# Kernel tuning notes

Measured on AMD Instinct MI355X. Metric: run time of the kernel, lower is better.

## Reference

```python
import jax, jax.numpy as jnp
import numpy as np
from jax import lax

K = 8  # number of KNN neighbors (excluding self)


def setup_inputs() -> dict:
    key = jax.random.key(0)
    k1, k2, k3 = jax.random.split(key, 3)
    B, H, W, C = 32, 14, 14, 2048
    OUT = 512
    x = jax.random.normal(k1, (B, H, W, C), dtype=jnp.float32)
    W1 = jax.random.normal(k2, (C, OUT), dtype=jnp.float32) * (1.0 / np.sqrt(C))
    b1 = jnp.zeros((OUT,), dtype=jnp.float32)
    W2 = jax.random.normal(k3, (OUT, OUT), dtype=jnp.float32) * (1.0 / np.sqrt(OUT))
    b2 = jnp.zeros((OUT,), dtype=jnp.float32)
    return {"x": x, "W1": W1, "b1": b1, "W2": W2, "b2": b2}


def _knn_edges(xf, k):
    # full pairwise squared-euclidean distance (monotone in cdist p=2)
    sq = jnp.sum(xf * xf, axis=-1)                      # [N]
    d2 = sq[:, None] + sq[None, :] - 2.0 * (xf @ xf.T)  # [N, N]
    _, idx = lax.top_k(-d2, k + 1)                      # smallest k+1
    knn = idx[:, 1:]                                    # drop self
    N = xf.shape[0]
    src = jnp.repeat(jnp.arange(N), k)
    dst = knn.reshape(-1)
    # GCNConv adds self-loops
    loops = jnp.arange(N)
    src = jnp.concatenate([src, loops])
    dst = jnp.concatenate([dst, loops])
    return src, dst


def _gcn_conv(h, W, b, src, dst, N):
    # PyG GCNConv: sym-normalized aggregation with self-loops
    deg = jax.ops.segment_sum(jnp.ones_like(dst, dtype=h.dtype), dst, num_segments=N)
    dinv = lax.rsqrt(jnp.maximum(deg, 1.0))
    norm = dinv[src] * dinv[dst]                        # [E]
    hw = h @ W                                          # [N, F]
    msg = hw[src] * norm[:, None]                       # gather + scale
    out = jax.ops.segment_sum(msg, dst, num_segments=N) # scatter-add
    return out + b


def reference(x, W1, b1, W2, b2):
    B, H, Wd, C = x.shape
    N = B * H * Wd
    xf = x.reshape(N, C)
    src, dst = _knn_edges(xf, K)
    h = jax.nn.relu(_gcn_conv(xf, W1, b1, src, dst, N))
    # dropout is identity in eval mode
    h = jax.nn.relu(_gcn_conv(h, W2, b2, src, dst, N))
    return h.reshape(B, H, Wd, W2.shape[1])
```

## Files before the change

### kernel.cpp

```cpp
#include <hip/hip_runtime.h>

typedef __attribute__((ext_vector_type(8))) _Float16 half8;
typedef __attribute__((ext_vector_type(4))) _Float16 half4;
typedef __attribute__((ext_vector_type(4))) float f32x4;

#define N_NODES 6272
#define CDIM    2048
#define ODIM    512
#define NPAN    49
#define NSLOT   392
#define GRID_G  1232
#define GRID_H1 392
#define E2      0.5f

#define XHI_OFF    0ul
#define CANDV_OFF  25690112ul
#define CANDI_OFF  35524608ul
#define SQ_OFF     40441856ul
#define KNN_OFF    40466944ul
#define DINV_OFF   41520640ul
#define RPTR_OFF   41545728ul
#define COL_OFF    41571072ul
#define W1T_OFF    41796864ul
#define W2T_OFF    43894016ul
#define H1H_OFF    44418304ul
#define HW_OFF     50843648ul

__device__ __forceinline__ void gld_lds16(const void* g, void* l) {
    __builtin_amdgcn_global_load_lds(
        (const __attribute__((address_space(1))) void*)g,
        (__attribute__((address_space(3))) void*)l, 16, 0, 0);
}

__device__ __forceinline__ half8 frag_read(const char* base, int row, int s, int lane) {
    int b = (s * 4 + (lane >> 4)) ^ (row & 7);
    return *(const half8*)(base + row * 128 + b * 16);
}

#define MF(a, b, c) __builtin_amdgcn_mfma_f32_16x16x32_f16(a, b, c, 0, 0, 0)

__global__ __launch_bounds__(256) void prep_kernel(const float* __restrict__ x,
        _Float16* __restrict__ xhi, float* __restrict__ sq,
        const float* __restrict__ W1, _Float16* __restrict__ w1t,
        const float* __restrict__ W2, _Float16* __restrict__ w2t) {
    __shared__ float tile[64][65];
    int bid = blockIdx.x, tid = threadIdx.x;
    if (bid < 1568) {
        int i = bid * 4 + (tid >> 6);
        int t = tid & 63;
        const float* row = x + (size_t)i * CDIM;
        _Float16* hrow = xhi + (size_t)i * CDIM;
        float s = 0.f;
#pragma unroll
        for (int k = 0; k < 8; k++) {
            float4 v = *(const float4*)(row + (k * 64 + t) * 4);
            half4 h;
            h[0] = (_Float16)v.x; h[1] = (_Float16)v.y;
            h[2] = (_Float16)v.z; h[3] = (_Float16)v.w;
            *(half4*)(hrow + (k * 64 + t) * 4) = h;
            s += v.x * v.x + v.y * v.y + v.z * v.z + v.w * v.w;
        }
#pragma unroll
        for (int off = 32; off; off >>= 1) s += __shfl_down(s, off, 64);
        if (t == 0) sq[i] = s;
        return;
    }
    const float* W; _Float16* Wt; int K, N, idx;
    if (bid < 1824) { idx = bid - 1568; W = W1; Wt = w1t; K = CDIM; N = ODIM; }
    else            { idx = bid - 1824; W = W2; Wt = w2t; K = ODIM; N = ODIM; }
    int nkb = K / 64;
    int kb = (idx % nkb) * 64, nb = (idx / nkb) * 64;
    int r = tid >> 2, c0 = (tid & 3) * 16;
#pragma unroll
    for (int u = 0; u < 4; u++) {
        float4 v = *(const float4*)(W + (size_t)(kb + r) * N + nb + c0 + u * 4);
        tile[r][c0 + u * 4 + 0] = v.x; tile[r][c0 + u * 4 + 1] = v.y;
        tile[r][c0 + u * 4 + 2] = v.z; tile[r][c0 + u * 4 + 3] = v.w;
    }
    __syncthreads();
    int rn = tid >> 2, ck0 = (tid & 3) * 16;
#pragma unroll
    for (int u = 0; u < 4; u++) {
        half4 o;
#pragma unroll
        for (int j = 0; j < 4; j++) o[j] = (_Float16)tile[ck0 + u * 4 + j][rn];
        *(half4*)(Wt + (size_t)(nb + rn) * K + kb + ck0 + u * 4) = o;
    }
}

__global__ __launch_bounds__(256, 4) void gram_hgemm_kernel(
        const _Float16* __restrict__ xhi, const float* __restrict__ sq,
        float* __restrict__ candv, unsigned short* __restrict__ candi,
        const _Float16* __restrict__ w1t, _Float16* __restrict__ hw) {
    __shared__ char lds[32768];
    int tid = threadIdx.x, lane = tid & 63, wave = tid >> 6;
    int l15 = lane & 15, kg = lane >> 4;
    int r_in = lane >> 3;
    int skb = (lane & 7) ^ r_in;

    if (blockIdx.x >= GRID_G) {
        int hb = blockIdx.x - GRID_G;
        const int nit = N_NODES / 64;
        int per = GRID_H1 >> 3;
        int swz = (hb & 7) * per + (hb >> 3);
        int i0 = (swz % nit) * 64, j0 = (swz / nit) * 128;
        f32x4 acc[4][2] = {};
#pragma unroll 1
        for (int kk = 0; kk < CDIM; kk += 64) {
            __syncthreads();
#pragma unroll
            for (int g = 0; g < 6; g++) {
                int sg = wave * 6 + g;
                if (sg < 8) {
                    gld_lds16(xhi + (size_t)(i0 + sg * 8 + r_in) * CDIM + kk + skb * 8,
                              lds + sg * 1024);
                } else {
                    int seg = sg - 8;
                    gld_lds16(w1t + (size_t)(j0 + seg * 8 + r_in) * CDIM + kk + skb * 8,
                              lds + 8192 + seg * 1024);
                }
            }
            __syncthreads();
#pragma unroll
            for (int s = 0; s < 2; s++) {
                half8 a[4];
#pragma unroll
                for (int m = 0; m < 4; m++) a[m] = frag_read(lds, m * 16 + l15, s, lane);
#pragma unroll
                for (int n = 0; n < 2; n++) {
                    half8 b = frag_read(lds + 8192, wave * 32 + n * 16 + l15, s, lane);
#pragma unroll
                    for (int m = 0; m < 4; m++) acc[m][n] = MF(a[m], b, acc[m][n]);
                }
            }
        }
#pragma unroll
        for (int m = 0; m < 4; m++)
#pragma unroll
            for (int n = 0; n < 2; n++)
#pragma unroll
                for (int r = 0; r < 4; r++) {
                    int row = i0 + m * 16 + kg * 4 + r;
                    int colj = j0 + wave * 32 + n * 16 + l15;
                    hw[(size_t)row * ODIM + colj] = (_Float16)acc[m][n][r];
                }
        return;
    }

    float* S = (float*)lds;
    float* topv = (float*)(lds + 16896);
    unsigned short* topi = (unsigned short*)(lds + 21504);
#define TOPV(r, k) topv[(r) * 9 + (k)]
#define TOPI(r, k) topi[(r) * 10 + (k)]
    int wr = wave >> 1, wc = wave & 1;

    int xcd = blockIdx.x & 7, loc = blockIdx.x >> 3;
    if (xcd != 0 && loc >= 153) return;
    int raster = (xcd == 0) ? loc : (154 + (xcd - 1) * 153 + loc);
    int t = (int)((sqrtf(8.f * (float)raster + 1.f) - 1.f) * 0.5f);
    while ((t + 1) * (t + 2) / 2 <= raster) t++;
    while (t * (t + 1) / 2 > raster) t--;
    int p = raster - t * (t + 1) / 2;
    size_t i0 = (size_t)p * 128, j0 = (size_t)t * 128;

    f32x4 acc[4][4] = {};

#pragma unroll 1
    for (int c = 0; c < 32; c++) {
        int kk = c * 64;
#pragma unroll
        for (int g = 0; g < 8; g++) {
            int sg = wave * 8 + g;
            int tI = sg >> 4, seg = sg & 15;
            size_t row = (tI ? j0 : i0) + (size_t)(seg * 8 + r_in);
            gld_lds16(xhi + row * CDIM + kk + skb * 8, lds + tI * 16384 + seg * 1024);
        }
        __syncthreads();
#pragma unroll
        for (int s = 0; s < 2; s++) {
            half8 a4[4];
#pragma unroll
            for (int m = 0; m < 4; m++)
                a4[m] = frag_read(lds, wr * 64 + m * 16 + l15, s, lane);
#pragma unroll
            for (int n = 0; n < 4; n++) {
                half8 b = frag_read(lds + 16384, wc * 64 + n * 16 + l15, s, lane);
#pragma unroll
                for (int m = 0; m < 4; m++) acc[m][n] = MF(a4[m], b, acc[m][n]);
            }
        }
        __syncthreads();
    }

    float sqi[4][4];
#pragma unroll
    for (int m = 0; m < 4; m++)
#pragma unroll
        for (int r = 0; r < 4; r++)
            sqi[m][r] = sq[(int)i0 + wr * 64 + m * 16 + kg * 4 + r];
    float sqj[4];
#pragma unroll
    for (int n = 0; n < 4; n++)
        sqj[n] = sq[(int)j0 + wc * 64 + n * 16 + l15];

    if (tid < 128) {
#pragma unroll
        for (int k = 0; k < 8; k++) { TOPV(tid, k) = 3.4e38f; TOPI(tid, k) = 0xFFFF; }
    }

#pragma unroll
    for (int cs = 0; cs < 4; cs++) {
        __syncthreads();
        if (wc == (cs >> 1)) {
            const int n0 = (cs & 1) * 2;
#pragma unroll
            for (int m = 0; m < 4; m++)
#pragma unroll
                for (int nn = 0; nn < 2; nn++)
#pragma unroll
                    for (int r = 0; r < 4; r++) {
                        int row = wr * 64 + m * 16 + kg * 4 + r;
                        float d2 = sqi[m][r] + sqj[n0 + nn] - 2.f * acc[m][n0 + nn][r];
                        S[row * 33 + nn * 16 + l15] = d2;
                    }
        }
        __syncthreads();
        if (tid < 128) {
            int r = tid, gi = (int)i0 + r;
            int cbase = (int)j0 + cs * 32;
#pragma unroll 4
            for (int jj = 0; jj < 32; jj++) {
                int gj = cbase + jj;
                if (gj == gi) continue;
                float v = S[r * 33 + jj];
                float wv = TOPV(r, 7); int wi = TOPI(r, 7);
                if (v < wv || (v == wv && gj < wi)) {
                    int pos = 7;
                    while (pos > 0) {
                        float pv = TOPV(r, pos - 1); int pi = TOPI(r, pos - 1);
                        if (v < pv || (v == pv && gj < pi)) {
                            TOPV(r, pos) = pv; TOPI(r, pos) = (unsigned short)pi; pos--;
                        } else break;
                    }
                    TOPV(r, pos) = v; TOPI(r, pos) = (unsigned short)gj;
                }
            }
        }
    }
    __syncthreads();
    if (tid < 128) {
        int gi = (int)i0 + tid;
#pragma unroll
        for (int k = 0; k < 8; k++) {
            candv[(size_t)gi * NSLOT + t * 8 + k] = TOPV(tid, k);
            candi[(size_t)gi * NSLOT + t * 8 + k] = TOPI(tid, k);
        }
#pragma unroll
        for (int k = 0; k < 8; k++) { TOPV(tid, k) = 3.4e38f; TOPI(tid, k) = 0xFFFF; }
    }

    if (p < t) {
#pragma unroll
        for (int ss = 0; ss < 4; ss++) {
            __syncthreads();
            if (wr == (ss >> 1)) {
                const int mb = (ss & 1) * 2;
#pragma unroll
                for (int mm = 0; mm < 2; mm++)
#pragma unroll
                    for (int n = 0; n < 4; n++)
#pragma unroll
                        for (int r = 0; r < 4; r++) {
                            int rl  = mm * 16 + kg * 4 + r;
                            int col = wc * 64 + n * 16 + l15;
                            float d2 = sqi[mb + mm][r] + sqj[n] - 2.f * acc[mb + mm][n][r];
                            S[col * 33 + rl] = d2;
                        }
            }
            __syncthreads();
            if (tid < 128) {
                int cc = tid;
                int rbase = (int)i0 + ss * 32;
#pragma unroll 4
                for (int jj = 0; jj < 32; jj++) {
                    int gi = rbase + jj;
                    float v = S[cc * 33 + jj];
                    float wv = TOPV(cc, 7); int wi = TOPI(cc, 7);
                    if (v < wv || (v == wv && gi < wi)) {
                        int pos = 7;
                        while (pos > 0) {
                            float pv = TOPV(cc, pos - 1); int pi = TOPI(cc, pos - 1);
                            if (v < pv || (v == pv && gi < pi)) {
                                TOPV(cc, pos) = pv; TOPI(cc, pos) = (unsigned short)pi; pos--;
                            } else break;
                        }
                        TOPV(cc, pos) = v; TOPI(cc, pos) = (unsigned short)gi;
                    }
                }
            }
        }
        __syncthreads();
        if (tid < 128) {
            int gj = (int)j0 + tid;
#pragma unroll
            for (int k = 0; k < 8; k++) {
                candv[(size_t)gj * NSLOT + p * 8 + k] = TOPV(tid, k);
                candi[(size_t)gj * NSLOT + p * 8 + k] = TOPI(tid, k);
            }
        }
    }
#undef TOPV
#undef TOPI
}

__global__ __launch_bounds__(256) void knn_select_kernel(
        const float* __restrict__ candv, const unsigned short* __restrict__ candi,
        const float* __restrict__ x, const float* __restrict__ sq,
        int* __restrict__ knn) {
    int node = blockIdx.x * 4 + (threadIdx.x >> 6);
    int lane = threadIdx.x & 63;
    const float* cv = candv + (size_t)node * NSLOT;
    const unsigned short* ci = candi + (size_t)node * NSLOT;
    float v[7]; int ix[7];
#pragma unroll
    for (int u = 0; u < 7; u++) {
        int s = u * 64 + lane;
        bool ok = (s < NSLOT);
        v[u]  = ok ? cv[s] : 3.4e38f;
        ix[u] = ok ? (int)ci[s] : 0x7fffffff;
    }
    float myv16 = 3.4e38f; int myc = 0x7fffffff;
#pragma unroll 1
    for (int k = 0; k < 16; k++) {
        float bv = v[0]; int bi = ix[0];
#pragma unroll
        for (int u = 1; u < 7; u++)
            if (v[u] < bv || (v[u] == bv && ix[u] < bi)) { bv = v[u]; bi = ix[u]; }
#pragma unroll
        for (int off = 32; off; off >>= 1) {
            float ov = __shfl_xor(bv, off, 64);
            int   oi = __shfl_xor(bi, off, 64);
            if (ov < bv || (ov == bv && oi < bi)) { bv = ov; bi = oi; }
        }
        if (lane == k) { myv16 = bv; myc = bi; }
#pragma unroll
        for (int u = 0; u < 7; u++)
            if (ix[u] == bi) { v[u] = 3.4e38f; ix[u] = 0x7fffffff; }
    }
    float v7 = __shfl(myv16, 7, 64), v8 = __shfl(myv16, 8, 64);
    if (v8 - v7 > E2) {
        if (lane < 8) knn[(size_t)node * 8 + lane] = myc;
        return;
    }
    bool isc  = (lane < 16);
    bool cin  = isc && (myv16 < v7 - E2);
    bool cout = isc && (myv16 > v8 + E2);
    bool band = isc && !cin && !cout;
    unsigned long long bm = __ballot(band);
    float fv = myv16;
    if (cin)  fv = myv16 - 1e9f;
    if (cout) fv = myv16 + 1e9f;

    const float* xi = x + (size_t)node * CDIM;
    float4 a[8];
#pragma unroll
    for (int g = 0; g < 8; g++) a[g] = *(const float4*)(xi + (g * 64 + lane) * 4);
    float sqi = sq[node];
#pragma unroll 1
    for (int c = 0; c < 16; c++) {
        if (!((bm >> c) & 1ull)) continue;
        int j = __shfl(myc, c, 64);
        const float* xj = x + (size_t)j * CDIM;
        float s = 0.f;
#pragma unroll
        for (int g = 0; g < 8; g++) {
            float4 b = *(const float4*)(xj + (g * 64 + lane) * 4);
            s = fmaf(a[g].x, b.x, s); s = fmaf(a[g].y, b.y, s);
            s = fmaf(a[g].z, b.z, s); s = fmaf(a[g].w, b.w, s);
        }
#pragma unroll
        for (int off = 32; off; off >>= 1) s += __shfl_down(s, off, 64);
        float d2 = sqi + sq[j] - 2.f * s;
        d2 = __shfl(d2, 0, 64);
        if (lane == c) fv = d2;
    }
    float rv = (lane < 16) ? fv : 3.4e38f;
    int   ri = (lane < 16) ? myc : 0x7fffffff;
#pragma unroll 1
    for (int k = 0; k < 8; k++) {
        float bv = rv; int bi = ri;
#pragma unroll
        for (int off = 8; off; off >>= 1) {
            float ov = __shfl_xor(bv, off, 64);
            int   oi = __shfl_xor(bi, off, 64);
            if (ov < bv || (ov == bv && oi < bi)) { bv = ov; bi = oi; }
        }
        bv = __shfl(bv, lane & 15, 64); bi = __shfl(bi, lane & 15, 64);
        if (lane == 0) knn[(size_t)node * 8 + k] = bi;
        if (ri == bi) { rv = 3.4e38f; ri = 0x7fffffff; }
    }
}

__global__ __launch_bounds__(1024) void graph_build_kernel(
        const int* __restrict__ knn, float* __restrict__ dinv,
        int* __restrict__ row_ptr, int* __restrict__ col) {
    __shared__ int deg_l[N_NODES];
    __shared__ int cnt_l[N_NODES];
    __shared__ int rp_l[N_NODES];
    __shared__ int partial[1024];
    int tid = threadIdx.x;
    for (int i = tid; i < N_NODES; i += 1024) { deg_l[i] = 1; cnt_l[i] = 0; }
    __syncthreads();
    for (int e = tid; e < N_NODES * 8; e += 1024) atomicAdd(&deg_l[knn[e]], 1);
    __syncthreads();
    const int CH = 7;
    int start = tid * CH;
    int end = start + CH; if (end > N_NODES) end = N_NODES;
    int s = 0;
    for (int i = start; i < end; i++) s += deg_l[i];
    partial[tid] = s;
    __syncthreads();
    if (tid == 0) {
        int run = 0;
        for (int k = 0; k < 1024; k++) { int vv = partial[k]; partial[k] = run; run += vv; }
        row_ptr[N_NODES] = run;
    }
    __syncthreads();
    int run = partial[tid];
    for (int i = start; i < end; i++) {
        rp_l[i] = run; row_ptr[i] = run;
        dinv[i] = rsqrtf((float)deg_l[i]);
        run += deg_l[i];
    }
    __syncthreads();
    for (int i = tid; i < N_NODES; i += 1024) {
        int p0 = rp_l[i] + atomicAdd(&cnt_l[i], 1);
        col[p0] = i;
#pragma unroll
        for (int j = 0; j < 8; j++) {
            int d = knn[i * 8 + j];
            int q = rp_l[d] + atomicAdd(&cnt_l[d], 1);
            col[q] = i;
        }
    }
}

__global__ __launch_bounds__(256) void hgemm_nt_kernel(
        const _Float16* __restrict__ A, const _Float16* __restrict__ Bt,
        _Float16* __restrict__ C, int M, int N, int K) {
    __shared__ char lds[24576];
    int tid = threadIdx.x, lane = tid & 63, wave = tid >> 6;
    int l15 = lane & 15, kg = lane >> 4;
    int nt = N >> 7;
    int nblk = (M >> 6) * nt;
    int per = nblk >> 3;
    int swz = (blockIdx.x & 7) * per + (blockIdx.x >> 3);
    int i0 = (swz % (M >> 6)) * 64, j0 = (swz / (M >> 6)) * 128;
    f32x4 acc[4][2] = {};

    int r_in = lane >> 3;
    int skb = (lane & 7) ^ r_in;

#pragma unroll 1
    for (int kk = 0; kk < K; kk += 64) {
        __syncthreads();
#pragma unroll
        for (int g = 0; g < 6; g++) {
            int sg = wave * 6 + g;
            if (sg < 8) {
                gld_lds16(A + (size_t)(i0 + sg * 8 + r_in) * K + kk + skb * 8,
                          lds + sg * 1024);
            } else {
                int seg = sg - 8;
                gld_lds16(Bt + (size_t)(j0 + seg * 8 + r_in) * K + kk + skb * 8,
                          lds + 8192 + seg * 1024);
            }
        }
        __syncthreads();
#pragma unroll
        for (int s = 0; s < 2; s++) {
            half8 a[4];
#pragma unroll
            for (int m = 0; m < 4; m++) a[m] = frag_read(lds, m * 16 + l15, s, lane);
#pragma unroll
            for (int n = 0; n < 2; n++) {
                half8 b = frag_read(lds + 8192, wave * 32 + n * 16 + l15, s, lane);
#pragma unroll
                for (int m = 0; m < 4; m++) acc[m][n] = MF(a[m], b, acc[m][n]);
            }
        }
    }
#pragma unroll
    for (int m = 0; m < 4; m++)
#pragma unroll
        for (int n = 0; n < 2; n++)
#pragma unroll
            for (int r = 0; r < 4; r++) {
                int row = i0 + m * 16 + kg * 4 + r;
                int colj = j0 + wave * 32 + n * 16 + l15;
                C[(size_t)row * N + colj] = (_Float16)acc[m][n][r];
            }
}

template <bool HALF_OUT>
__global__ __launch_bounds__(256) void aggregate_kernel(
        const _Float16* __restrict__ hw, const int* __restrict__ row_ptr,
        const int* __restrict__ col, const float* __restrict__ dinv,
        const float* __restrict__ bias, void* __restrict__ outp) {
    int node = blockIdx.x * 4 + (threadIdx.x >> 6);
    int lane = threadIdx.x & 63;
    int e0 = row_ptr[node], e1 = row_ptr[node + 1];
    float acc[8] = {};
    for (int e = e0; e < e1; e++) {
        int s = col[e];
        float w = dinv[s];
        half8 v = *(const half8*)(hw + (size_t)s * ODIM + lane * 8);
#pragma unroll
        for (int j = 0; j < 8; j++) acc[j] = fmaf(w, (float)v[j], acc[j]);
    }
    float wd = dinv[node];
    float4 b0 = *(const float4*)(bias + lane * 8);
    float4 b1 = *(const float4*)(bias + lane * 8 + 4);
    float o[8];
    o[0] = fmaxf(fmaf(acc[0], wd, b0.x), 0.f);
    o[1] = fmaxf(fmaf(acc[1], wd, b0.y), 0.f);
    o[2] = fmaxf(fmaf(acc[2], wd, b0.z), 0.f);
    o[3] = fmaxf(fmaf(acc[3], wd, b0.w), 0.f);
    o[4] = fmaxf(fmaf(acc[4], wd, b1.x), 0.f);
    o[5] = fmaxf(fmaf(acc[5], wd, b1.y), 0.f);
    o[6] = fmaxf(fmaf(acc[6], wd, b1.z), 0.f);
    o[7] = fmaxf(fmaf(acc[7], wd, b1.w), 0.f);
    if (HALF_OUT) {
        half8 h;
#pragma unroll
        for (int j = 0; j < 8; j++) h[j] = (_Float16)o[j];
        *(half8*)((_Float16*)outp + (size_t)node * ODIM + lane * 8) = h;
    } else {
        float* out = (float*)outp;
        float4 f0 = {o[0], o[1], o[2], o[3]}, f1 = {o[4], o[5], o[6], o[7]};
        *(float4*)(out + (size_t)node * ODIM + lane * 8)     = f0;
        *(float4*)(out + (size_t)node * ODIM + lane * 8 + 4) = f1;
    }
}

extern "C" void kernel_launch(void* const* d_in, const int* in_sizes, int n_in,
                              void* d_out, int out_size, void* d_ws, size_t ws_size,
                              hipStream_t stream) {
    const float* x  = (const float*)d_in[0];
    const float* W1 = (const float*)d_in[1];
    const float* b1 = (const float*)d_in[2];
    const float* W2 = (const float*)d_in[3];
    const float* b2 = (const float*)d_in[4];
    float* out = (float*)d_out;
    char* ws = (char*)d_ws;

    _Float16* xhi  = (_Float16*)(ws + XHI_OFF);
    float* candv   = (float*)(ws + CANDV_OFF);
    unsigned short* candi = (unsigned short*)(ws + CANDI_OFF);
    float* sq      = (float*)(ws + SQ_OFF);
    int*   knn     = (int*)  (ws + KNN_OFF);
    float* dinv    = (float*)(ws + DINV_OFF);
    int*   row_ptr = (int*)  (ws + RPTR_OFF);
    int*   col     = (int*)  (ws + COL_OFF);
    _Float16* w1t  = (_Float16*)(ws + W1T_OFF);
    _Float16* w2t  = (_Float16*)(ws + W2T_OFF);
    _Float16* hw   = (_Float16*)(ws + HW_OFF);
    _Float16* h1h  = (_Float16*)(ws + H1H_OFF);

    prep_kernel<<<1888, 256, 0, stream>>>(x, xhi, sq, W1, w1t, W2, w2t);
    gram_hgemm_kernel<<<GRID_G + GRID_H1, 256, 0, stream>>>(xhi, sq, candv, candi, w1t, hw);
    knn_select_kernel<<<N_NODES / 4, 256, 0, stream>>>(candv, candi, x, sq, knn);
    graph_build_kernel<<<1, 1024, 0, stream>>>(knn, dinv, row_ptr, col);

    aggregate_kernel<true><<<N_NODES / 4, 256, 0, stream>>>(hw, row_ptr, col, dinv, b1, (void*)h1h);
    hgemm_nt_kernel<<<(N_NODES / 64) * (ODIM / 128), 256, 0, stream>>>(h1h, w2t, hw, N_NODES, ODIM, ODIM);
    aggregate_kernel<false><<<N_NODES / 4, 256, 0, stream>>>(hw, row_ptr, col, dinv, b2, (void*)out);
}
```

Baseline: 1.079 ms.

## Split single-block graph build into multi-block init, degree, scan and scatter kernels

Replaces the one-block graph construction kernel with four kernels: degree init, degree counting with global atomics across many blocks, a single-block scan computing row pointers and dinv, and a multi-block CSR scatter. This is meant to remove the serialization of all edge atomics and the scatter onto one workgroup. The cost is three extra launches and global rather than LDS atomics.

```diff
diff --git a/kernel.cpp b/kernel.cpp
--- a/kernel.cpp
+++ b/kernel.cpp
@@ -18,6 +18,8 @@
 #define CANDI_OFF  35524608ul
 #define SQ_OFF     40441856ul
 #define KNN_OFF    40466944ul
+#define CNT_OFF    40667648ul
+#define DEG_OFF    40692736ul
 #define DINV_OFF   41520640ul
 #define RPTR_OFF   41545728ul
 #define COL_OFF    41571072ul
@@ -401,23 +403,24 @@
     }
 }
 
-__global__ __launch_bounds__(1024) void graph_build_kernel(
-        const int* __restrict__ knn, float* __restrict__ dinv,
-        int* __restrict__ row_ptr, int* __restrict__ col) {
-    __shared__ int deg_l[N_NODES];
-    __shared__ int cnt_l[N_NODES];
-    __shared__ int rp_l[N_NODES];
+__global__ __launch_bounds__(256) void graph_init_kernel(int* deg, int* cnt) {
+    int i = blockIdx.x * 256 + threadIdx.x;
+    if (i < N_NODES) { deg[i] = 1; cnt[i] = 0; }
+}
+__global__ __launch_bounds__(256) void deg_count_kernel(const int* __restrict__ knn,
+                                                        int* deg) {
+    int e = blockIdx.x * 256 + threadIdx.x;
+    if (e < N_NODES * 8) atomicAdd(&deg[knn[e]], 1);
+}
+__global__ __launch_bounds__(1024) void scan_dinv_kernel(const int* __restrict__ deg,
+        float* __restrict__ dinv, int* __restrict__ row_ptr) {
     __shared__ int partial[1024];
+    const int CH = 7;
     int tid = threadIdx.x;
-    for (int i = tid; i < N_NODES; i += 1024) { deg_l[i] = 1; cnt_l[i] = 0; }
-    __syncthreads();
-    for (int e = tid; e < N_NODES * 8; e += 1024) atomicAdd(&deg_l[knn[e]], 1);
-    __syncthreads();
-    const int CH = 7;
     int start = tid * CH;
     int end = start + CH; if (end > N_NODES) end = N_NODES;
     int s = 0;
-    for (int i = start; i < end; i++) s += deg_l[i];
+    for (int i = start; i < end; i++) s += deg[i];
     partial[tid] = s;
     __syncthreads();
     if (tid == 0) {
@@ -428,20 +431,22 @@
     __syncthreads();
     int run = partial[tid];
     for (int i = start; i < end; i++) {
-        rp_l[i] = run; row_ptr[i] = run;
-        dinv[i] = rsqrtf((float)deg_l[i]);
-        run += deg_l[i];
-    }
-    __syncthreads();
-    for (int i = tid; i < N_NODES; i += 1024) {
-        int p0 = rp_l[i] + atomicAdd(&cnt_l[i], 1);
-        col[p0] = i;
-#pragma unroll
-        for (int j = 0; j < 8; j++) {
-            int d = knn[i * 8 + j];
-            int q = rp_l[d] + atomicAdd(&cnt_l[d], 1);
-            col[q] = i;
-        }
+        row_ptr[i] = run;
+        dinv[i] = rsqrtf((float)deg[i]);
+        run += deg[i];
+    }
+}
+__global__ __launch_bounds__(256) void scatter_kernel(const int* __restrict__ knn,
+        const int* __restrict__ row_ptr, int* cnt, int* __restrict__ col) {
+    int i = blockIdx.x * 256 + threadIdx.x;
+    if (i >= N_NODES) return;
+    int p0 = row_ptr[i] + atomicAdd(&cnt[i], 1);
+    col[p0] = i;
+#pragma unroll
+    for (int j = 0; j < 8; j++) {
+        int d = knn[(size_t)i * 8 + j];
+        int q = row_ptr[d] + atomicAdd(&cnt[d], 1);
+        col[q] = i;
     }
 }
 
@@ -559,6 +564,8 @@
     unsigned short* candi = (unsigned short*)(ws + CANDI_OFF);
     float* sq      = (float*)(ws + SQ_OFF);
     int*   knn     = (int*)  (ws + KNN_OFF);
+    int*   cnt     = (int*)  (ws + CNT_OFF);
+    int*   deg     = (int*)  (ws + DEG_OFF);
     float* dinv    = (float*)(ws + DINV_OFF);
     int*   row_ptr = (int*)  (ws + RPTR_OFF);
     int*   col     = (int*)  (ws + COL_OFF);
@@ -570,7 +577,11 @@
     prep_kernel<<<1888, 256, 0, stream>>>(x, xhi, sq, W1, w1t, W2, w2t);
     gram_hgemm_kernel<<<GRID_G + GRID_H1, 256, 0, stream>>>(xhi, sq, candv, candi, w1t, hw);
     knn_select_kernel<<<N_NODES / 4, 256, 0, stream>>>(candv, candi, x, sq, knn);
-    graph_build_kernel<<<1, 1024, 0, stream>>>(knn, dinv, row_ptr, col);
+
+    graph_init_kernel<<<(N_NODES + 255) / 256, 256, 0, stream>>>(deg, cnt);
+    deg_count_kernel<<<(N_NODES * 8) / 256, 256, 0, stream>>>(knn, deg);
+    scan_dinv_kernel<<<1, 1024, 0, stream>>>(deg, dinv, row_ptr);
+    scatter_kernel<<<(N_NODES + 255) / 256, 256, 0, stream>>>(knn, row_ptr, cnt, col);
 
     aggregate_kernel<true><<<N_NODES / 4, 256, 0, stream>>>(hw, row_ptr, col, dinv, b1, (void*)h1h);
     hgemm_nt_kernel<<<(N_NODES / 64) * (ODIM / 128), 256, 0, stream>>>(h1h, w2t, hw, N_NODES, ODIM, ODIM);
```

Result: no change. 1.081 ms (+0.2%).
